# Optimization experiments

Hardware: AMD Instinct MI355X
Metric: run time of the kernel (lower is better)

Reference implementation:

```python
import jax, jax.numpy as jnp
import numpy as np

IMG = 640
C = 80
K = 10
LB, LC = 7.5, 0.5
ALPHA_COST, BETA_COST = 0.5, 6.0
GAMMA, ALPHA = 2.0, 0.25
EPS = 1e-7
PI = 3.141592653589793


def xywh_to_xyxy(b):
    cx, cy, w, h = b[..., 0], b[..., 1], b[..., 2], b[..., 3]
    return jnp.stack([cx - w * 0.5, cy - h * 0.5, cx + w * 0.5, cy + h * 0.5], axis=-1)


def bbox_iou(box1, box2):
    # box1 [M,4], box2 [N,4] xyxy -> [M,N]
    area1 = jnp.clip(box1[:, 2] - box1[:, 0], 0) * jnp.clip(box1[:, 3] - box1[:, 1], 0)
    area2 = jnp.clip(box2[:, 2] - box2[:, 0], 0) * jnp.clip(box2[:, 3] - box2[:, 1], 0)
    ix1 = jnp.maximum(box1[:, None, 0], box2[None, :, 0])
    iy1 = jnp.maximum(box1[:, None, 1], box2[None, :, 1])
    ix2 = jnp.minimum(box1[:, None, 2], box2[None, :, 2])
    iy2 = jnp.minimum(box1[:, None, 3], box2[None, :, 3])
    inter = jnp.clip(ix2 - ix1, 0) * jnp.clip(iy2 - iy1, 0)
    union = area1[:, None] + area2[None, :] - inter + EPS
    return jnp.clip(inter / union, 0.0, 1.0)


def bbox_ciou(p, t):
    # elementwise [N,4] x [N,4] xyxy -> [N]
    px1, py1, px2, py2 = p[:, 0], p[:, 1], p[:, 2], p[:, 3]
    tx1, ty1, tx2, ty2 = t[:, 0], t[:, 1], t[:, 2], t[:, 3]
    pw = jnp.clip(px2 - px1, EPS)
    ph = jnp.clip(py2 - py1, EPS)
    tw = jnp.clip(tx2 - tx1, EPS)
    th = jnp.clip(ty2 - ty1, EPS)
    inter = jnp.clip(jnp.minimum(px2, tx2) - jnp.maximum(px1, tx1), 0) * \
            jnp.clip(jnp.minimum(py2, ty2) - jnp.maximum(py1, ty1), 0)
    union = pw * ph + tw * th - inter + EPS
    iou = inter / union
    cd = ((px1 + px2) * 0.5 - (tx1 + tx2) * 0.5) ** 2 + ((py1 + py2) * 0.5 - (ty1 + ty2) * 0.5) ** 2
    cw = jnp.maximum(px2, tx2) - jnp.minimum(px1, tx1)
    ch = jnp.maximum(py2, ty2) - jnp.minimum(py1, ty1)
    c2 = cw ** 2 + ch ** 2 + EPS
    v = (4.0 / PI ** 2) * (jnp.arctan(tw / th) - jnp.arctan(pw / ph)) ** 2
    alpha = jax.lax.stop_gradient(v / (v - iou + 1.0 + EPS))
    return iou - cd / c2 - alpha * v


def _decode(p, stride):
    # p: [B, A, S, S, E] -> box [B, A*S*S, 4] (xywh px), cls [B, A*S*S, C]
    B, A, S, _, E = p.shape
    tx, ty, tw, th = p[..., 0], p[..., 1], p[..., 2], p[..., 3]
    gy, gx = jnp.meshgrid(jnp.arange(S, dtype=p.dtype), jnp.arange(S, dtype=p.dtype), indexing='ij')
    gx = gx.reshape(1, 1, S, S)
    gy = gy.reshape(1, 1, S, S)
    px = (jax.nn.sigmoid(tx) * 2.0 - 0.5 + gx) * stride  # center_mode='v8'
    py = (jax.nn.sigmoid(ty) * 2.0 - 0.5 + gy) * stride
    pw = jax.nn.softplus(tw) * stride                      # wh_mode='softplus'
    ph = jax.nn.softplus(th) * stride
    box = jnp.stack([px, py, pw, ph], axis=-1).reshape(B, -1, 4)
    cls = p[..., 4:].reshape(B, -1, C)
    return box, cls


def _per_image(p_box, p_logits, gt, labels):
    # p_box [M,4] xywh, p_logits [M,C], gt [N,4] xyxy, labels [N]
    N = gt.shape[0]
    tcx = (gt[:, 0] + gt[:, 2]) * 0.5
    tcy = (gt[:, 1] + gt[:, 3]) * 0.5
    dist = (p_box[:, 0][:, None] - tcx[None, :]) ** 2 + (p_box[:, 1][:, None] - tcy[None, :]) ** 2  # [M,N]
    _, cand = jax.lax.top_k(-dist.T, K)       # [N,K] nearest anchors per target
    cand = cand.reshape(-1)                    # [N*K] (dups don't change the min)
    cand_box = p_box[cand]
    cand_logits = p_logits[cand]
    cls_score = jax.nn.sigmoid(cand_logits)[:, labels]          # [NK,N]
    iou = bbox_iou(xywh_to_xyxy(cand_box), gt)                  # [NK,N]
    cost = ALPHA_COST * (1.0 - cls_score) + BETA_COST * (1.0 - iou)
    matched = cand[jnp.argmin(cost, axis=0)]                    # [N]
    ciou = bbox_ciou(xywh_to_xyxy(p_box[matched]), gt)
    loss_box = LB * jnp.sum(1.0 - ciou) / N
    tgt = jnp.zeros_like(p_logits).at[matched, labels].set(1.0)  # [M,C]
    x = p_logits
    ce = jnp.maximum(x, 0) - x * tgt + jnp.log1p(jnp.exp(-jnp.abs(x)))
    pr = jax.nn.sigmoid(x)
    p_t = pr * tgt + (1 - pr) * (1 - tgt)
    fl = ce * (1 - p_t) ** GAMMA
    a_t = ALPHA * tgt + (1 - ALPHA) * (1 - tgt)
    loss_cls = LC * jnp.sum(a_t * fl) / N
    return loss_box + loss_cls


def _forward(p0, p1, p2, gt_boxes, labels):
    boxes, logits = [], []
    for p in (p0, p1, p2):
        S = p.shape[2]
        pb, pl = _decode(p, float(IMG) / S)
        boxes.append(pb)
        logits.append(pl)
    flat_boxes = jnp.concatenate(boxes, axis=1)    # [B, 8400, 4]
    flat_logits = jnp.concatenate(logits, axis=1)  # [B, 8400, C]
    per_img = jax.vmap(_per_image)(flat_boxes, flat_logits, gt_boxes, labels)  # [B]
    return jnp.mean(per_img)


def setup_inputs() -> dict:
    key = jax.random.key(0)
    k0, k1, k2, kc, kw, kl = jax.random.split(key, 6)
    B, N = 16, 60
    p0 = jax.random.normal(k0, (B, 1, 80, 80, 84), dtype=jnp.float32)
    p1 = jax.random.normal(k1, (B, 1, 40, 40, 84), dtype=jnp.float32)
    p2 = jax.random.normal(k2, (B, 1, 20, 20, 84), dtype=jnp.float32)
    c = jax.random.uniform(kc, (B, N, 2), minval=64.0, maxval=576.0)
    wh = jax.random.uniform(kw, (B, N, 2), minval=8.0, maxval=128.0)
    gt_boxes = jnp.concatenate([c - wh * 0.5, c + wh * 0.5], axis=-1).astype(jnp.float32)
    labels = jax.random.randint(kl, (B, N), 0, 80, dtype=jnp.int32)
    return {"p0": p0, "p1": p1, "p2": p2, "gt_boxes": gt_boxes, "labels": labels}


def reference(p0, p1, p2, gt_boxes, labels):
    return _forward(p0, p1, p2, gt_boxes, labels)
```

## Files before the change

### kernel.cpp

```cpp
#include <hip/hip_runtime.h>
#include <cfloat>
#include <math.h>

#define NB   16
#define NGT  60
#define NA   8400
#define KNN  10
#define NCAND (NGT*KNN)
#define EPSF 1e-7f
#define PIF  3.14159265358979f
#define FOCAL_BLOCKS 2048

#define NV0   2150400u
#define NV1    537600u
#define NV2    134400u
#define NVTOT 2822400u
#define NROWS  134400u
#define FOCAL_COUNT 2688000u

#define LOG2E 1.44269504088896341f
#define LN2   0.69314718055994531f

__device__ __forceinline__ float fexp2(float x){ return __builtin_amdgcn_exp2f(x); }
__device__ __forceinline__ float flog2(float x){ return __builtin_amdgcn_logf(x); }
__device__ __forceinline__ float frcp (float x){ return __builtin_amdgcn_rcpf(x); }

__device__ __forceinline__ float fsigm(float x){
  return frcp(1.0f + fexp2(-x*LOG2E));
}
__device__ __forceinline__ float fsoftplus(float x){
  float u = fexp2(-fabsf(x)*LOG2E);
  return fmaxf(x,0.f) + LN2*flog2(1.0f + u);
}
__device__ __forceinline__ float fbg(float x){
  float u = fexp2(fminf(-x*LOG2E, 126.0f));
  float t = frcp(1.0f + u);
  return (x + LN2*flog2(1.0f + u)) * t * t;
}

template<int S, int BASE, int STRIDE_I>
__device__ __forceinline__ void decode_row(const float* __restrict__ p, unsigned row,
                                           float4* __restrict__ boxes){
  unsigned img   = row / (unsigned)(S*S);
  unsigned local = row - img*(unsigned)(S*S);
  unsigned i = local / (unsigned)S, j = local - i*(unsigned)S;
  float4 x4 = *(const float4*)(p + (size_t)row*84u);
  const float stf = (float)STRIDE_I;
  float px = (fsigm(x4.x)*2.f - 0.5f + (float)j)*stf;
  float py = (fsigm(x4.y)*2.f - 0.5f + (float)i)*stf;
  float pw = fsoftplus(x4.z)*stf;
  float ph = fsoftplus(x4.w)*stf;
  boxes[(size_t)img*NA + BASE + local] = make_float4(px,py,pw,ph);
}

__global__ __launch_bounds__(256) void fused_decode_focal(const float* __restrict__ p0,
                                                          const float* __restrict__ p1,
                                                          const float* __restrict__ p2,
                                                          float4* __restrict__ boxes,
                                                          float* __restrict__ fsum){
  __shared__ float sbuf[4];
  float sum = 0.f;
  unsigned stride = gridDim.x*blockDim.x;
  for (unsigned u = blockIdx.x*blockDim.x + threadIdx.x; u < NVTOT; u += stride){
    if (u < FOCAL_COUNT){
      unsigned g = u / 20u;
      unsigned v = 21u*g + (u - 20u*g) + 1u;
      const float* p; unsigned vloc;
      if (v < NV0)           { p=p0; vloc = v; }
      else if (v < NV0+NV1)  { p=p1; vloc = v - NV0; }
      else                   { p=p2; vloc = v - (NV0+NV1); }
      float4 x4 = *(const float4*)(p + (size_t)vloc*4u);
      sum += fbg(x4.x) + fbg(x4.y) + fbg(x4.z) + fbg(x4.w);
    } else {
      unsigned row = u - FOCAL_COUNT;
      if (row < 102400u)      decode_row<80,    0,  8>(p0, row,           boxes);
      else if (row < 128000u) decode_row<40, 6400, 16>(p1, row - 102400u, boxes);
      else                    decode_row<20, 8000, 32>(p2, row - 128000u, boxes);
    }
  }
  sum *= 0.75f;
  #pragma unroll
  for (int off=32; off>0; off>>=1) sum += __shfl_xor(sum, off);
  int wid = threadIdx.x >> 6;
  if ((threadIdx.x & 63) == 0) sbuf[wid] = sum;
  __syncthreads();
  if (threadIdx.x == 0) fsum[blockIdx.x] = sbuf[0]+sbuf[1]+sbuf[2]+sbuf[3];
}

__device__ __forceinline__ const float* anchor_base(const float* p0,const float* p1,const float* p2,int img,int a){
  if (a < 6400) return p0 + (size_t)(img*6400 + a)*84;
  if (a < 8000) return p1 + (size_t)(img*1600 + (a-6400))*84;
  return p2 + (size_t)(img*400 + (a-8000))*84;
}

__global__ __launch_bounds__(256) void topk_kernel(const float4* __restrict__ boxes,
                                                   const float* __restrict__ gt,
                                                   int* __restrict__ cand){
  int wid  = threadIdx.x >> 6;
  int lane = threadIdx.x & 63;
  int pair = blockIdx.x*4 + wid;
  int img = pair / NGT, g = pair - img*NGT;
  const float* gb = gt + (size_t)(img*NGT + g)*4;
  float tcx = (gb[0]+gb[2])*0.5f, tcy = (gb[1]+gb[3])*0.5f;

  int jx0 = (int)(tcx * 0.125f),   iy0 = (int)(tcy * 0.125f);
  int jx1 = (int)(tcx * 0.0625f),  iy1 = (int)(tcy * 0.0625f);
  int jx2 = (int)(tcx * 0.03125f), iy2 = (int)(tcy * 0.03125f);

  const float4* bb = boxes + (size_t)img*NA;

  float d0=FLT_MAX,d1=FLT_MAX,d2=FLT_MAX,d3=FLT_MAX;
  int   a0,a1,a2,a3;
  #pragma unroll
  for (int s=0; s<4; s++){
    int c = lane + 64*s;
    float dd = FLT_MAX; int aa = 9000000 + c;
    int i, j, S, base, valid = 1;
    if (c < 169)      { int r=c/13,  q=c-13*r;           i=iy0-6+r; j=jx0-6+q; S=80; base=0; }
    else if (c < 218) { int t=c-169; int r=t/7, q=t-7*r; i=iy1-3+r; j=jx1-3+q; S=40; base=6400; }
    else if (c < 243) { int t=c-218; int r=t/5, q=t-5*r; i=iy2-2+r; j=jx2-2+q; S=20; base=8000; }
    else { valid = 0; i=j=0; S=1; base=0; }
    if (valid && i>=0 && i<S && j>=0 && j<S){
      int anchor = base + i*S + j;
      float4 b = bb[anchor];
      float dx=b.x-tcx, dy=b.y-tcy;
      dd = dx*dx + dy*dy;
      aa = anchor;
    }
    if (s==0){ d0=dd; a0=aa; } else if (s==1){ d1=dd; a1=aa; }
    else if (s==2){ d2=dd; a2=aa; } else { d3=dd; a3=aa; }
  }

  for (int r=0; r<KNN; r++){
    float v = d0; int anc = a0;
    if (d1 < v || (d1==v && a1<anc)){ v=d1; anc=a1; }
    if (d2 < v || (d2==v && a2<anc)){ v=d2; anc=a2; }
    if (d3 < v || (d3==v && a3<anc)){ v=d3; anc=a3; }
    #pragma unroll
    for (int off=32; off>0; off>>=1){
      float v2 = __shfl_xor(v, off);
      int  A2 = __shfl_xor(anc, off);
      if (v2 < v || (v2==v && A2<anc)){ v=v2; anc=A2; }
    }
    if (a0==anc) d0=FLT_MAX;
    if (a1==anc) d1=FLT_MAX;
    if (a2==anc) d2=FLT_MAX;
    if (a3==anc) d3=FLT_MAX;
    if (lane == 0) cand[(size_t)pair*KNN + r] = anc;
  }
}

__global__ __launch_bounds__(256) void match_kernel(const float4* __restrict__ boxes,
                                                    const int* __restrict__ cand,
                                                    const float* __restrict__ gt,
                                                    const int* __restrict__ labels,
                                                    const float* __restrict__ p0,
                                                    const float* __restrict__ p1,
                                                    const float* __restrict__ p2,
                                                    int* __restrict__ matched){
  int pair = blockIdx.x;
  int img = pair / NGT, j = pair - img*NGT;
  int tid = threadIdx.x;
  int wid = tid >> 6, lane = tid & 63;
  const float* gb = gt + (size_t)(img*NGT + j)*4;
  float gx=gb[0], gy=gb[1], gz=gb[2], gw=gb[3];
  float a2 = fmaxf(gz-gx,0.f)*fmaxf(gw-gy,0.f);
  int lab = labels[img*NGT + j];

  const int* ci = cand + (size_t)img*NCAND;
  float best = FLT_MAX; int bslot = 1<<30; int banchor = -1;
  for (int c=tid; c<NCAND; c+=256){
    int a = ci[c];
    float4 b = boxes[(size_t)img*NA + a];
    float bx1=b.x-b.z*0.5f, by1=b.y-b.w*0.5f, bx2=b.x+b.z*0.5f, by2=b.y+b.w*0.5f;
    float a1 = fmaxf(bx2-bx1,0.f)*fmaxf(by2-by1,0.f);
    float ix1=fmaxf(bx1,gx), iy1=fmaxf(by1,gy);
    float ix2=fminf(bx2,gz), iy2=fminf(by2,gw);
    float inter = fmaxf(ix2-ix1,0.f)*fmaxf(iy2-iy1,0.f);
    float uni = a1 + a2 - inter + EPSF;
    float iou = fminf(fmaxf(inter/uni,0.f),1.f);
    float lg = anchor_base(p0,p1,p2,img,a)[4+lab];
    float cost = 0.5f*(1.f - fsigm(lg)) + 6.f*(1.f - iou);
    if (cost < best){ best=cost; bslot=c; banchor=a; }
  }
  #pragma unroll
  for (int off=32; off>0; off>>=1){
    float v2 = __shfl_xor(best, off);
    int  s2 = __shfl_xor(bslot, off);
    int  a2s= __shfl_xor(banchor, off);
    if (v2 < best || (v2==best && s2<bslot)){ best=v2; bslot=s2; banchor=a2s; }
  }
  __shared__ float bc[4]; __shared__ int bs[4], ba[4];
  if (lane == 0){ bc[wid]=best; bs[wid]=bslot; ba[wid]=banchor; }
  __syncthreads();
  if (tid == 0){
    float v=bc[0]; int s=bs[0]; int a=ba[0];
    #pragma unroll
    for (int k=1;k<4;k++){
      if (bc[k] < v || (bc[k]==v && bs[k]<s)){ v=bc[k]; s=bs[k]; a=ba[k]; }
    }
    matched[img*NGT + j] = a;
  }
}

__global__ __launch_bounds__(1024) void tail_kernel(const float4* __restrict__ boxes,
                                                    const int* __restrict__ matched_g,
                                                    const float* __restrict__ gt,
                                                    const int* __restrict__ labels,
                                                    const float* __restrict__ p0,
                                                    const float* __restrict__ p1,
                                                    const float* __restrict__ p2,
                                                    const float* __restrict__ fsum,
                                                    float* __restrict__ out){
  int tid = threadIdx.x;
  int wid = tid >> 6;
  int lane = tid & 63;
  __shared__ int sm[NB][NGT];
  __shared__ int sl[NB][NGT];
  __shared__ float wb[NB], wc[NB], wf[NB];
  if (lane < NGT){
    sm[wid][lane] = matched_g[wid*NGT + lane];
    sl[wid][lane] = labels[wid*NGT + lane];
  }
  __syncthreads();

  int img = wid;
  float local_box = 0.f, local_corr = 0.f;
  if (lane < NGT){
    int j = lane;
    int m = sm[img][j];
    float4 pb = boxes[(size_t)img*NA + m];
    float px1=pb.x-pb.z*0.5f, py1=pb.y-pb.w*0.5f, px2=pb.x+pb.z*0.5f, py2=pb.y+pb.w*0.5f;
    const float* gb = gt + (size_t)(img*NGT + j)*4;
    float gx=gb[0], gy=gb[1], gz=gb[2], gw=gb[3];
    float pw=fmaxf(px2-px1,EPSF), ph=fmaxf(py2-py1,EPSF);
    float tw=fmaxf(gz-gx,EPSF),  th=fmaxf(gw-gy,EPSF);
    float inter = fmaxf(fminf(px2,gz)-fmaxf(px1,gx),0.f)*fmaxf(fminf(py2,gw)-fmaxf(py1,gy),0.f);
    float uni = pw*ph + tw*th - inter + EPSF;
    float iou = inter/uni;
    float dcx = (px1+px2)*0.5f - (gx+gz)*0.5f;
    float dcy = (py1+py2)*0.5f - (gy+gw)*0.5f;
    float cd = dcx*dcx + dcy*dcy;
    float cw = fmaxf(px2,gz) - fminf(px1,gx);
    float ch = fmaxf(py2,gw) - fminf(py1,gy);
    float c2 = cw*cw + ch*ch + EPSF;
    float dv = atanf(tw/th) - atanf(pw/ph);
    float v  = (4.f/(PIF*PIF))*dv*dv;
    float alpha = v/(v - iou + 1.f + EPSF);
    float ciou = iou - cd/c2 - alpha*v;
    local_box = 1.f - ciou;

    int lab = sl[img][j];
    bool dup = false;
    for (int j2=0; j2<j; j2++)
      if (sm[img][j2]==m && sl[img][j2]==lab){ dup=true; break; }
    if (!dup){
      float x = anchor_base(p0,p1,p2,img,m)[4+lab];
      float s  = fsigm(x);
      float u  = fexp2(-fabsf(x)*LOG2E);
      float lt = LN2*flog2(1.0f + u);
      float sp_pos = fmaxf(-x,0.f) + lt;
      float sp_neg = fmaxf( x,0.f) + lt;
      local_corr = 0.25f*sp_pos*(1.f-s)*(1.f-s) - 0.75f*sp_neg*s*s;
    }
  }
  float local_f = fsum[tid] + fsum[tid + 1024];
  #pragma unroll
  for (int off=32; off>0; off>>=1){
    local_box  += __shfl_xor(local_box,  off);
    local_corr += __shfl_xor(local_corr, off);
    local_f    += __shfl_xor(local_f,    off);
  }
  if (lane == 0){ wb[wid]=local_box; wc[wid]=local_corr; wf[wid]=local_f; }
  __syncthreads();
  if (tid == 0){
    float sb=0.f, sc=0.f, sf=0.f;
    #pragma unroll
    for (int k=0;k<NB;k++){ sb+=wb[k]; sc+=wc[k]; sf+=wf[k]; }
    out[0] = (7.5f*sb + 0.5f*(sf + sc)) / (60.f*16.f);
  }
}

extern "C" void kernel_launch(void* const* d_in, const int* in_sizes, int n_in,
                              void* d_out, int out_size, void* d_ws, size_t ws_size,
                              hipStream_t stream){
  const float* p0 = (const float*)d_in[0];
  const float* p1 = (const float*)d_in[1];
  const float* p2 = (const float*)d_in[2];
  const float* gt = (const float*)d_in[3];
  const int* labels = (const int*)d_in[4];
  float* out = (float*)d_out;

  float4* boxes   = (float4*)d_ws;
  int*    cand    = (int*)((char*)d_ws + (size_t)NB*NA*sizeof(float4));
  int*    matched = (int*)((char*)cand + (size_t)NB*NCAND*sizeof(int));
  float*  fsum    = (float*)((char*)matched + (size_t)NB*NGT*sizeof(int));

  fused_decode_focal<<<FOCAL_BLOCKS, 256, 0, stream>>>(p0, p1, p2, boxes, fsum);
  topk_kernel<<<NB*NGT/4, 256, 0, stream>>>(boxes, gt, cand);
  match_kernel<<<NB*NGT, 256, 0, stream>>>(boxes, cand, gt, labels, p0, p1, p2, matched);
  tail_kernel<<<1, 1024, 0, stream>>>(boxes, matched, gt, labels, p0, p1, p2, fsum, out);
}
```

Before: 46.47 us.

## Drop materialized box buffer; decode boxes on demand and fuse topk into focal kernel

Removes the decode pass that wrote all 134400 boxes to workspace. Box decoding now happens inline wherever a box is needed: topk reads only the xy logits of its local window, and match and tail decode their candidate anchors directly. The topk work runs as extra blocks inside the focal reduction launch, which removes one kernel launch and its dependency. The cost is recomputed sigmoid and softplus per candidate, plus scattered reads of the 84-float rows.

```diff
diff --git a/kernel.cpp b/kernel.cpp
--- a/kernel.cpp
+++ b/kernel.cpp
@@ -10,12 +10,11 @@
 #define EPSF 1e-7f
 #define PIF  3.14159265358979f
 #define FOCAL_BLOCKS 2048
+#define TOPK_BLOCKS  240
 
 #define NV0   2150400u
 #define NV1    537600u
 #define NV2    134400u
-#define NVTOT 2822400u
-#define NROWS  134400u
 #define FOCAL_COUNT 2688000u
 
 #define LOG2E 1.44269504088896341f
@@ -38,45 +37,98 @@
   return (x + LN2*flog2(1.0f + u)) * t * t;
 }
 
-template<int S, int BASE, int STRIDE_I>
-__device__ __forceinline__ void decode_row(const float* __restrict__ p, unsigned row,
-                                           float4* __restrict__ boxes){
-  unsigned img   = row / (unsigned)(S*S);
-  unsigned local = row - img*(unsigned)(S*S);
-  unsigned i = local / (unsigned)S, j = local - i*(unsigned)S;
-  float4 x4 = *(const float4*)(p + (size_t)row*84u);
-  const float stf = (float)STRIDE_I;
-  float px = (fsigm(x4.x)*2.f - 0.5f + (float)j)*stf;
-  float py = (fsigm(x4.y)*2.f - 0.5f + (float)i)*stf;
-  float pw = fsoftplus(x4.z)*stf;
-  float ph = fsoftplus(x4.w)*stf;
-  boxes[(size_t)img*NA + BASE + local] = make_float4(px,py,pw,ph);
-}
-
-__global__ __launch_bounds__(256) void fused_decode_focal(const float* __restrict__ p0,
-                                                          const float* __restrict__ p1,
-                                                          const float* __restrict__ p2,
-                                                          float4* __restrict__ boxes,
-                                                          float* __restrict__ fsum){
+struct ARow { const float* q; float stf; int i, j; };
+__device__ __forceinline__ ARow anchor_row(const float* p0,const float* p1,const float* p2,int img,int a){
+  ARow r;
+  if (a < 6400){ int l=a;      r.q = p0 + (size_t)(img*6400 + l)*84; r.stf= 8.f; r.i=l/80; r.j=l-80*r.i; }
+  else if (a < 8000){ int l=a-6400; r.q = p1 + (size_t)(img*1600 + l)*84; r.stf=16.f; r.i=l/40; r.j=l-40*r.i; }
+  else { int l=a-8000;         r.q = p2 + (size_t)(img*400  + l)*84; r.stf=32.f; r.i=l/20; r.j=l-20*r.i; }
+  return r;
+}
+__device__ __forceinline__ float4 decode_box_xywh(const ARow& r){
+  float4 x4 = *(const float4*)r.q;
+  float px = (fsigm(x4.x)*2.f - 0.5f + (float)r.j)*r.stf;
+  float py = (fsigm(x4.y)*2.f - 0.5f + (float)r.i)*r.stf;
+  float pw = fsoftplus(x4.z)*r.stf;
+  float ph = fsoftplus(x4.w)*r.stf;
+  return make_float4(px,py,pw,ph);
+}
+
+__global__ __launch_bounds__(256) void focal_topk_kernel(const float* __restrict__ p0,
+                                                         const float* __restrict__ p1,
+                                                         const float* __restrict__ p2,
+                                                         const float* __restrict__ gt,
+                                                         int* __restrict__ cand,
+                                                         float* __restrict__ fsum){
+  if (blockIdx.x < TOPK_BLOCKS){
+    int wid  = threadIdx.x >> 6;
+    int lane = threadIdx.x & 63;
+    int pair = blockIdx.x*4 + wid;
+    int img = pair / NGT, g = pair - img*NGT;
+    const float* gb = gt + (size_t)(img*NGT + g)*4;
+    float tcx = (gb[0]+gb[2])*0.5f, tcy = (gb[1]+gb[3])*0.5f;
+
+    int jx0 = (int)(tcx * 0.125f),   iy0 = (int)(tcy * 0.125f);
+    int jx1 = (int)(tcx * 0.0625f),  iy1 = (int)(tcy * 0.0625f);
+    int jx2 = (int)(tcx * 0.03125f), iy2 = (int)(tcy * 0.03125f);
+
+    float d0=FLT_MAX,d1=FLT_MAX,d2=FLT_MAX,d3=FLT_MAX;
+    int   a0,a1,a2,a3;
+    #pragma unroll
+    for (int s=0; s<4; s++){
+      int c = lane + 64*s;
+      float dd = FLT_MAX; int aa = 9000000 + c;
+      const float* p; int i, j, S, base, rowmul, valid = 1; float stf;
+      if (c < 169)      { int r=c/13,  q=c-13*r;           i=iy0-6+r; j=jx0-6+q; S=80; base=0;    p=p0; rowmul=6400; stf= 8.f; }
+      else if (c < 218) { int t=c-169; int r=t/7, q=t-7*r; i=iy1-3+r; j=jx1-3+q; S=40; base=6400; p=p1; rowmul=1600; stf=16.f; }
+      else if (c < 243) { int t=c-218; int r=t/5, q=t-5*r; i=iy2-2+r; j=jx2-2+q; S=20; base=8000; p=p2; rowmul=400;  stf=32.f; }
+      else { valid = 0; i=j=0; S=1; base=0; p=p0; rowmul=0; stf=0.f; }
+      if (valid && i>=0 && i<S && j>=0 && j<S){
+        int local = i*S + j;
+        const float* q4 = p + (size_t)(img*rowmul + local)*84u;
+        float2 xy = *(const float2*)q4;
+        float px = (fsigm(xy.x)*2.f - 0.5f + (float)j)*stf;
+        float py = (fsigm(xy.y)*2.f - 0.5f + (float)i)*stf;
+        float dx=px-tcx, dy=py-tcy;
+        dd = dx*dx + dy*dy;
+        aa = base + local;
+      }
+      if (s==0){ d0=dd; a0=aa; } else if (s==1){ d1=dd; a1=aa; }
+      else if (s==2){ d2=dd; a2=aa; } else { d3=dd; a3=aa; }
+    }
+
+    for (int r=0; r<KNN; r++){
+      float v = d0; int anc = a0;
+      if (d1 < v || (d1==v && a1<anc)){ v=d1; anc=a1; }
+      if (d2 < v || (d2==v && a2<anc)){ v=d2; anc=a2; }
+      if (d3 < v || (d3==v && a3<anc)){ v=d3; anc=a3; }
+      #pragma unroll
+      for (int off=32; off>0; off>>=1){
+        float v2 = __shfl_xor(v, off);
+        int  A2 = __shfl_xor(anc, off);
+        if (v2 < v || (v2==v && A2<anc)){ v=v2; anc=A2; }
+      }
+      if (a0==anc) d0=FLT_MAX;
+      if (a1==anc) d1=FLT_MAX;
+      if (a2==anc) d2=FLT_MAX;
+      if (a3==anc) d3=FLT_MAX;
+      if (lane == 0) cand[(size_t)pair*KNN + r] = anc;
+    }
+    return;
+  }
+
   __shared__ float sbuf[4];
   float sum = 0.f;
-  unsigned stride = gridDim.x*blockDim.x;
-  for (unsigned u = blockIdx.x*blockDim.x + threadIdx.x; u < NVTOT; u += stride){
-    if (u < FOCAL_COUNT){
-      unsigned g = u / 20u;
-      unsigned v = 21u*g + (u - 20u*g) + 1u;
-      const float* p; unsigned vloc;
-      if (v < NV0)           { p=p0; vloc = v; }
-      else if (v < NV0+NV1)  { p=p1; vloc = v - NV0; }
-      else                   { p=p2; vloc = v - (NV0+NV1); }
-      float4 x4 = *(const float4*)(p + (size_t)vloc*4u);
-      sum += fbg(x4.x) + fbg(x4.y) + fbg(x4.z) + fbg(x4.w);
-    } else {
-      unsigned row = u - FOCAL_COUNT;
-      if (row < 102400u)      decode_row<80,    0,  8>(p0, row,           boxes);
-      else if (row < 128000u) decode_row<40, 6400, 16>(p1, row - 102400u, boxes);
-      else                    decode_row<20, 8000, 32>(p2, row - 128000u, boxes);
-    }
+  const unsigned stride = FOCAL_BLOCKS*256u;
+  for (unsigned u = (blockIdx.x - TOPK_BLOCKS)*256u + threadIdx.x; u < FOCAL_COUNT; u += stride){
+    unsigned g = u / 20u;
+    unsigned v = 21u*g + (u - 20u*g) + 1u;
+    const float* p; unsigned vloc;
+    if (v < NV0)           { p=p0; vloc = v; }
+    else if (v < NV0+NV1)  { p=p1; vloc = v - NV0; }
+    else                   { p=p2; vloc = v - (NV0+NV1); }
+    float4 x4 = *(const float4*)(p + (size_t)vloc*4u);
+    sum += fbg(x4.x) + fbg(x4.y) + fbg(x4.z) + fbg(x4.w);
   }
   sum *= 0.75f;
   #pragma unroll
@@ -84,74 +136,10 @@
   int wid = threadIdx.x >> 6;
   if ((threadIdx.x & 63) == 0) sbuf[wid] = sum;
   __syncthreads();
-  if (threadIdx.x == 0) fsum[blockIdx.x] = sbuf[0]+sbuf[1]+sbuf[2]+sbuf[3];
-}
-
-__device__ __forceinline__ const float* anchor_base(const float* p0,const float* p1,const float* p2,int img,int a){
-  if (a < 6400) return p0 + (size_t)(img*6400 + a)*84;
-  if (a < 8000) return p1 + (size_t)(img*1600 + (a-6400))*84;
-  return p2 + (size_t)(img*400 + (a-8000))*84;
-}
-
-__global__ __launch_bounds__(256) void topk_kernel(const float4* __restrict__ boxes,
-                                                   const float* __restrict__ gt,
-                                                   int* __restrict__ cand){
-  int wid  = threadIdx.x >> 6;
-  int lane = threadIdx.x & 63;
-  int pair = blockIdx.x*4 + wid;
-  int img = pair / NGT, g = pair - img*NGT;
-  const float* gb = gt + (size_t)(img*NGT + g)*4;
-  float tcx = (gb[0]+gb[2])*0.5f, tcy = (gb[1]+gb[3])*0.5f;
-
-  int jx0 = (int)(tcx * 0.125f),   iy0 = (int)(tcy * 0.125f);
-  int jx1 = (int)(tcx * 0.0625f),  iy1 = (int)(tcy * 0.0625f);
-  int jx2 = (int)(tcx * 0.03125f), iy2 = (int)(tcy * 0.03125f);
-
-  const float4* bb = boxes + (size_t)img*NA;
-
-  float d0=FLT_MAX,d1=FLT_MAX,d2=FLT_MAX,d3=FLT_MAX;
-  int   a0,a1,a2,a3;
-  #pragma unroll
-  for (int s=0; s<4; s++){
-    int c = lane + 64*s;
-    float dd = FLT_MAX; int aa = 9000000 + c;
-    int i, j, S, base, valid = 1;
-    if (c < 169)      { int r=c/13,  q=c-13*r;           i=iy0-6+r; j=jx0-6+q; S=80; base=0; }
-    else if (c < 218) { int t=c-169; int r=t/7, q=t-7*r; i=iy1-3+r; j=jx1-3+q; S=40; base=6400; }
-    else if (c < 243) { int t=c-218; int r=t/5, q=t-5*r; i=iy2-2+r; j=jx2-2+q; S=20; base=8000; }
-    else { valid = 0; i=j=0; S=1; base=0; }
-    if (valid && i>=0 && i<S && j>=0 && j<S){
-      int anchor = base + i*S + j;
-      float4 b = bb[anchor];
-      float dx=b.x-tcx, dy=b.y-tcy;
-      dd = dx*dx + dy*dy;
-      aa = anchor;
-    }
-    if (s==0){ d0=dd; a0=aa; } else if (s==1){ d1=dd; a1=aa; }
-    else if (s==2){ d2=dd; a2=aa; } else { d3=dd; a3=aa; }
-  }
-
-  for (int r=0; r<KNN; r++){
-    float v = d0; int anc = a0;
-    if (d1 < v || (d1==v && a1<anc)){ v=d1; anc=a1; }
-    if (d2 < v || (d2==v && a2<anc)){ v=d2; anc=a2; }
-    if (d3 < v || (d3==v && a3<anc)){ v=d3; anc=a3; }
-    #pragma unroll
-    for (int off=32; off>0; off>>=1){
-      float v2 = __shfl_xor(v, off);
-      int  A2 = __shfl_xor(anc, off);
-      if (v2 < v || (v2==v && A2<anc)){ v=v2; anc=A2; }
-    }
-    if (a0==anc) d0=FLT_MAX;
-    if (a1==anc) d1=FLT_MAX;
-    if (a2==anc) d2=FLT_MAX;
-    if (a3==anc) d3=FLT_MAX;
-    if (lane == 0) cand[(size_t)pair*KNN + r] = anc;
-  }
-}
-
-__global__ __launch_bounds__(256) void match_kernel(const float4* __restrict__ boxes,
-                                                    const int* __restrict__ cand,
+  if (threadIdx.x == 0) fsum[blockIdx.x - TOPK_BLOCKS] = sbuf[0]+sbuf[1]+sbuf[2]+sbuf[3];
+}
+
+__global__ __launch_bounds__(256) void match_kernel(const int* __restrict__ cand,
                                                     const float* __restrict__ gt,
                                                     const int* __restrict__ labels,
                                                     const float* __restrict__ p0,
@@ -171,7 +159,8 @@
   float best = FLT_MAX; int bslot = 1<<30; int banchor = -1;
   for (int c=tid; c<NCAND; c+=256){
     int a = ci[c];
-    float4 b = boxes[(size_t)img*NA + a];
+    ARow ar = anchor_row(p0,p1,p2,img,a);
+    float4 b = decode_box_xywh(ar);
     float bx1=b.x-b.z*0.5f, by1=b.y-b.w*0.5f, bx2=b.x+b.z*0.5f, by2=b.y+b.w*0.5f;
     float a1 = fmaxf(bx2-bx1,0.f)*fmaxf(by2-by1,0.f);
     float ix1=fmaxf(bx1,gx), iy1=fmaxf(by1,gy);
@@ -179,7 +168,7 @@
     float inter = fmaxf(ix2-ix1,0.f)*fmaxf(iy2-iy1,0.f);
     float uni = a1 + a2 - inter + EPSF;
     float iou = fminf(fmaxf(inter/uni,0.f),1.f);
-    float lg = anchor_base(p0,p1,p2,img,a)[4+lab];
+    float lg = ar.q[4+lab];
     float cost = 0.5f*(1.f - fsigm(lg)) + 6.f*(1.f - iou);
     if (cost < best){ best=cost; bslot=c; banchor=a; }
   }
@@ -203,8 +192,7 @@
   }
 }
 
-__global__ __launch_bounds__(1024) void tail_kernel(const float4* __restrict__ boxes,
-                                                    const int* __restrict__ matched_g,
+__global__ __launch_bounds__(1024) void tail_kernel(const int* __restrict__ matched_g,
                                                     const float* __restrict__ gt,
                                                     const int* __restrict__ labels,
                                                     const float* __restrict__ p0,
@@ -229,7 +217,8 @@
   if (lane < NGT){
     int j = lane;
     int m = sm[img][j];
-    float4 pb = boxes[(size_t)img*NA + m];
+    ARow ar = anchor_row(p0,p1,p2,img,m);
+    float4 pb = decode_box_xywh(ar);
     float px1=pb.x-pb.z*0.5f, py1=pb.y-pb.w*0.5f, px2=pb.x+pb.z*0.5f, py2=pb.y+pb.w*0.5f;
     const float* gb = gt + (size_t)(img*NGT + j)*4;
     float gx=gb[0], gy=gb[1], gz=gb[2], gw=gb[3];
@@ -255,7 +244,7 @@
     for (int j2=0; j2<j; j2++)
       if (sm[img][j2]==m && sl[img][j2]==lab){ dup=true; break; }
     if (!dup){
-      float x = anchor_base(p0,p1,p2,img,m)[4+lab];
+      float x = ar.q[4+lab];
       float s  = fsigm(x);
       float u  = fexp2(-fabsf(x)*LOG2E);
       float lt = LN2*flog2(1.0f + u);
@@ -291,13 +280,11 @@
   const int* labels = (const int*)d_in[4];
   float* out = (float*)d_out;
 
-  float4* boxes   = (float4*)d_ws;
-  int*    cand    = (int*)((char*)d_ws + (size_t)NB*NA*sizeof(float4));
-  int*    matched = (int*)((char*)cand + (size_t)NB*NCAND*sizeof(int));
-  float*  fsum    = (float*)((char*)matched + (size_t)NB*NGT*sizeof(int));
-
-  fused_decode_focal<<<FOCAL_BLOCKS, 256, 0, stream>>>(p0, p1, p2, boxes, fsum);
-  topk_kernel<<<NB*NGT/4, 256, 0, stream>>>(boxes, gt, cand);
-  match_kernel<<<NB*NGT, 256, 0, stream>>>(boxes, cand, gt, labels, p0, p1, p2, matched);
-  tail_kernel<<<1, 1024, 0, stream>>>(boxes, matched, gt, labels, p0, p1, p2, fsum, out);
-}
+  int*   cand    = (int*)d_ws;
+  int*   matched = (int*)((char*)cand + (size_t)NB*NCAND*sizeof(int));
+  float* fsum    = (float*)((char*)matched + (size_t)NB*NGT*sizeof(int));
+
+  focal_topk_kernel<<<TOPK_BLOCKS + FOCAL_BLOCKS, 256, 0, stream>>>(p0, p1, p2, gt, cand, fsum);
+  match_kernel<<<NB*NGT, 256, 0, stream>>>(cand, gt, labels, p0, p1, p2, matched);
+  tail_kernel<<<1, 1024, 0, stream>>>(matched, gt, labels, p0, p1, p2, fsum, out);
+}
```

Result: faster. 43.15 us (-7.2%).
